# Optimization experiments

Measured on AMD Instinct MI355X. Metric: run time of the kernel, lower is better.

The kernel has to match this reference:

```python
import jax, jax.numpy as jnp
import numpy as np

D_MODEL = 1024
N_HEADS = 16
SEQ = 2048
BATCH = 2
EPS = 1e-5


def layer_norm(x, g, b):
    mu = jnp.mean(x, axis=-1, keepdims=True)
    var = jnp.mean(jnp.square(x - mu), axis=-1, keepdims=True)
    return (x - mu) * jax.lax.rsqrt(var + EPS) * g + b


def setup_inputs() -> dict:
    key = jax.random.key(0)
    ks = jax.random.split(key, 10)
    D = D_MODEL
    s = lambda fan_in: 1.0 / np.sqrt(fan_in)
    return {
        "x": jax.random.normal(ks[0], (BATCH, SEQ, D), dtype=jnp.float32),
        # weights stored [in, out] (torch Linear is y = x @ W.T; equivalent math)
        "w_attn": jax.random.uniform(ks[1], (D, 3 * D), minval=-s(D), maxval=s(D), dtype=jnp.float32),
        "b_attn": jnp.zeros((3 * D,), jnp.float32),
        "w_proj": jax.random.uniform(ks[2], (D, D), minval=-s(D), maxval=s(D), dtype=jnp.float32),
        "b_proj": jnp.zeros((D,), jnp.float32),
        "ln1_g": jnp.ones((D,), jnp.float32),
        "ln1_b": jnp.zeros((D,), jnp.float32),
        "ln2_g": jnp.ones((D,), jnp.float32),
        "ln2_b": jnp.zeros((D,), jnp.float32),
        "w_fc1": jax.random.uniform(ks[3], (D, 4 * D), minval=-s(D), maxval=s(D), dtype=jnp.float32),
        "b_fc1": jnp.zeros((4 * D,), jnp.float32),
        "w_fc2": jax.random.uniform(ks[4], (4 * D, D), minval=-s(4 * D), maxval=s(4 * D), dtype=jnp.float32),
        "b_fc2": jnp.zeros((D,), jnp.float32),
    }


def reference(x, w_attn, b_attn, w_proj, b_proj, ln1_g, ln1_b, ln2_g, ln2_b, w_fc1, b_fc1, w_fc2, b_fc2):
    B, L, D = x.shape
    H = N_HEADS
    Dh = D // H

    # --- attention sublayer ---
    h = layer_norm(x, ln1_g, ln1_b)
    qkv = h @ w_attn + b_attn                      # [B, L, 3D]
    # SOURCE BUG (faithful): q, k, v are all taken from the k third.
    k = qkv[..., D:2 * D]
    kh = k.reshape(B, L, H, Dh).transpose(0, 2, 1, 3)   # [B, H, L, Dh]
    att = jnp.einsum('bhqd,bhkd->bhqk', kh, kh) / jnp.sqrt(jnp.float32(Dh))
    att = jax.nn.softmax(att, axis=-1)
    out = jnp.einsum('bhqk,bhkd->bhqd', att, kh)         # [B, H, L, Dh]
    out = out.transpose(0, 2, 1, 3).reshape(B, L, D)
    x = x + (out @ w_proj + b_proj)

    # --- feed-forward sublayer ---
    h = layer_norm(x, ln2_g, ln2_b)
    h = jax.nn.relu(h @ w_fc1 + b_fc1)
    x = x + (h @ w_fc2 + b_fc2)
    return x
```

## Files before the change

kernel.cpp:

```cpp
#include <hip/hip_runtime.h>


typedef __attribute__((ext_vector_type(8))) short s8v;
typedef __attribute__((ext_vector_type(4))) short s4v;
typedef __attribute__((ext_vector_type(4))) float f4v;

#define D_MODEL 1024
#define SEQ 2048
#define BATCH 2
#define NH 16
#define DH 64
#define MROWS (BATCH * SEQ)

#define KH_SCALE 0.42466088f
#define KH_ISCALE 2.3548200f

__device__ __forceinline__ float b2f(unsigned short u) {
  union { unsigned int i; float f; } v; v.i = ((unsigned int)u) << 16; return v.f;
}
__device__ __forceinline__ unsigned short f2b(float f) {
  unsigned int i = __builtin_bit_cast(unsigned int, f);
  unsigned int r = (i + 0x7fffu + ((i >> 16) & 1u)) >> 16;
  return (unsigned short)r;
}
__device__ __forceinline__ void async16(const void* g, void* l) {
  __builtin_amdgcn_global_load_lds(
      (const __attribute__((address_space(1))) unsigned int*)g,
      (__attribute__((address_space(3))) unsigned int*)l, 16, 0, 0);
}
__device__ __forceinline__ unsigned short cvt_b(float f) { return f2b(f); }
__device__ __forceinline__ unsigned short cvt_b(unsigned short u) { return u; }

__device__ __forceinline__ float xp2(float x) {
#if __has_builtin(__builtin_amdgcn_exp2f)
  return __builtin_amdgcn_exp2f(x);
#else
  return exp2f(x);
#endif
}

__device__ __forceinline__ s4v cvt4(float a, float b, float c, float d) {
  unsigned int lo, hi;
  asm("v_cvt_pk_bf16_f32 %0, %1, %2" : "=v"(lo) : "v"(a), "v"(b));
  asm("v_cvt_pk_bf16_f32 %0, %1, %2" : "=v"(hi) : "v"(c), "v"(d));
  union { unsigned long long u; s4v v; } u;
  u.u = ((unsigned long long)hi << 32) | (unsigned long long)lo;
  return u.v;
}

#if __has_builtin(__builtin_amdgcn_mfma_f32_16x16x16_bf16)
__device__ __forceinline__ f4v mfma16(s4v a, s4v b, f4v c) {
  return __builtin_amdgcn_mfma_f32_16x16x16_bf16(a, b, c, 0, 0, 0);
}
#elif __has_builtin(__builtin_amdgcn_mfma_f32_16x16x16bf16_1k)
__device__ __forceinline__ f4v mfma16(s4v a, s4v b, f4v c) {
  return __builtin_amdgcn_mfma_f32_16x16x16bf16_1k(a, b, c, 0, 0, 0);
}
#else
__device__ __forceinline__ f4v mfma16(s4v a, s4v b, f4v c) {
  s8v aa = {a[0], a[1], a[2], a[3], 0, 0, 0, 0};
  s8v bb = {b[0], b[1], b[2], b[3], 0, 0, 0, 0};
  return __builtin_amdgcn_mfma_f32_16x16x32_bf16(aa, bb, c, 0, 0, 0);
}
#endif

__device__ __forceinline__ int xcd_swz(int bidl, int nwg) {
  return (nwg & 7) ? bidl : ((bidl & 7) * (nwg >> 3) + (bidl >> 3));
}

__global__ __launch_bounds__(256) void ln_kernel(
    const float* __restrict__ x, const float* __restrict__ g,
    const float* __restrict__ bb, unsigned short* __restrict__ out) {
  int row = blockIdx.x;
  int t = threadIdx.x;
  const float* xr = x + (size_t)row * D_MODEL;
  float v[4];
  float s = 0.f, s2 = 0.f;
#pragma unroll
  for (int i = 0; i < 4; ++i) {
    float f = xr[t + 256 * i];
    v[i] = f; s += f; s2 += f * f;
  }
#pragma unroll
  for (int off = 1; off < 64; off <<= 1) {
    s += __shfl_xor(s, off, 64);
    s2 += __shfl_xor(s2, off, 64);
  }
  __shared__ float red[8];
  if ((t & 63) == 0) { red[t >> 6] = s; red[4 + (t >> 6)] = s2; }
  __syncthreads();
  s = red[0] + red[1] + red[2] + red[3];
  s2 = red[4] + red[5] + red[6] + red[7];
  float mu = s * (1.f / D_MODEL);
  float var = s2 * (1.f / D_MODEL) - mu * mu;
  float rstd = rsqrtf(var + 1e-5f);
#pragma unroll
  for (int i = 0; i < 4; ++i) {
    int c = t + 256 * i;
    float h = (v[i] - mu) * rstd * g[c] + bb[c];
    out[(size_t)row * D_MODEL + c] = f2b(h);
  }
}

template <typename T>
__global__ __launch_bounds__(256) void transpose_b(
    const T* __restrict__ src, unsigned short* __restrict__ dst,
    int srcStride, int dstStride, long long srcBatch, long long dstBatch) {
  __shared__ unsigned short tile[64][65];
  const T* s = src + (size_t)blockIdx.z * srcBatch;
  unsigned short* d = dst + (size_t)blockIdx.z * dstBatch;
  int n0 = blockIdx.x * 64, k0 = blockIdx.y * 64;
  for (int i = threadIdx.x; i < 4096; i += 256) {
    int k = i >> 6, n = i & 63;
    tile[k][n] = cvt_b(s[(size_t)(k0 + k) * srcStride + n0 + n]);
  }
  __syncthreads();
  for (int i = threadIdx.x; i < 4096; i += 256) {
    int n = i >> 6, k = i & 63;
    d[(size_t)(n0 + n) * dstStride + k0 + k] = tile[k][n];
  }
}

template <int RES, bool RELU, bool KH, int OUTF, int BM, int BN>
__global__ __launch_bounds__(256) void gemm_bt(
    const unsigned short* __restrict__ A, const unsigned short* __restrict__ Bt,
    const float* __restrict__ bias, const float* __restrict__ res,
    void* __restrict__ out, int M, int N, int K) {
  constexpr int MT = BM / 32;
  constexpr int NT = BN / 32;
  __shared__ __align__(16) unsigned short lsA[2][BM * 64];
  __shared__ __align__(16) unsigned short lsB[2][BN * 64];
  int tid = threadIdx.x;
  int lane = tid & 63, w = tid >> 6, quad = lane >> 4, l16 = lane & 15;
  int bidl = blockIdx.y * (int)gridDim.x + blockIdx.x;
  int swz = xcd_swz(bidl, (int)(gridDim.x * gridDim.y));
  int m0 = (swz / (int)gridDim.x) * BM, n0 = (swz % (int)gridDim.x) * BN;
  int wm = (w >> 1) * (BM / 2), wn = (w & 1) * (BN / 2);
  f4v acc[MT][NT] = {};

  auto stage = [&](int bsel, int ktE) {
#pragma unroll
    for (int i = 0; i < MT; ++i) {
      int cb = w * (BM * 2) + i * 64;
      int ci = cb + lane;
      int row = ci >> 3, c = ci & 7;
      int cs = c ^ (row & 7);
      async16(A + (size_t)(m0 + row) * K + ktE + cs * 8, &lsA[bsel][cb * 8]);
    }
#pragma unroll
    for (int i = 0; i < NT; ++i) {
      int cb = w * (BN * 2) + i * 64;
      int ci = cb + lane;
      int row = ci >> 3, c = ci & 7;
      int cs = c ^ (row & 7);
      async16(Bt + (size_t)(n0 + row) * K + ktE + cs * 8, &lsB[bsel][cb * 8]);
    }
  };

  stage(0, 0);
  int nK = K >> 6;
  for (int kt = 0; kt < nK; ++kt) {
    int b = kt & 1;
    if (kt + 1 < nK) {
      stage(b ^ 1, (kt + 1) << 6);
      if constexpr (MT + NT == 4)      asm volatile("s_waitcnt vmcnt(4)" ::: "memory");
      else if constexpr (MT + NT == 6) asm volatile("s_waitcnt vmcnt(6)" ::: "memory");
      else                             asm volatile("s_waitcnt vmcnt(8)" ::: "memory");
    } else {
      asm volatile("s_waitcnt vmcnt(0)" ::: "memory");
    }
    __builtin_amdgcn_sched_barrier(0);
    __builtin_amdgcn_s_barrier();
    __builtin_amdgcn_sched_barrier(0);
#pragma unroll
    for (int s = 0; s < 2; ++s) {
      s8v af[MT], bf[NT];
#pragma unroll
      for (int t = 0; t < MT; ++t) {
        int am = wm + t * 16 + l16;
        int ac = (s * 4 + quad) ^ (am & 7);
        af[t] = *(const s8v*)(&lsA[b][am * 64 + ac * 8]);
      }
#pragma unroll
      for (int t = 0; t < NT; ++t) {
        int bn = wn + t * 16 + l16;
        int bc = (s * 4 + quad) ^ (bn & 7);
        bf[t] = *(const s8v*)(&lsB[b][bn * 64 + bc * 8]);
      }
#pragma unroll
      for (int ti = 0; ti < MT; ++ti)
#pragma unroll
        for (int tj = 0; tj < NT; ++tj)
          acc[ti][tj] = __builtin_amdgcn_mfma_f32_16x16x32_bf16(
              af[ti], bf[tj], acc[ti][tj], 0, 0, 0);
    }
    asm volatile("s_waitcnt lgkmcnt(0)" ::: "memory");
    __builtin_amdgcn_sched_barrier(0);
    __builtin_amdgcn_s_barrier();
    __builtin_amdgcn_sched_barrier(0);
  }
#pragma unroll
  for (int tj = 0; tj < NT; ++tj) {
    int col = n0 + wn + tj * 16 + l16;
    float bv = bias[col];
#pragma unroll
    for (int ti = 0; ti < MT; ++ti) {
#pragma unroll
      for (int r = 0; r < 4; ++r) {
        int rowg = m0 + wm + ti * 16 + quad * 4 + r;
        float vv = acc[ti][tj][r] + bv;
        if (KH) vv *= KH_SCALE;
        if (RES == 2) vv += res[(size_t)rowg * N + col];
        if (RELU) vv = fmaxf(vv, 0.f);
        size_t oidx;
        if (KH) {
          int b2 = rowg >> 11, l = rowg & 2047, h = col >> 6, d = col & 63;
          oidx = (((size_t)(b2 * NH + h)) * SEQ + l) * DH + d;
        } else {
          oidx = (size_t)rowg * N + col;
        }
        if (OUTF == 0) ((unsigned short*)out)[oidx] = f2b(vv);
        else           ((float*)out)[oidx] = vv;
      }
    }
  }
}

__global__ __launch_bounds__(512, 2) void gemm256(
    const unsigned short* __restrict__ A, const unsigned short* __restrict__ Bt,
    const float* __restrict__ bias, unsigned short* __restrict__ out,
    bool relu, int M, int N, int K) {
  __shared__ __align__(16) unsigned short lsA[2][2][128 * 64];
  __shared__ __align__(16) unsigned short lsB[2][2][128 * 64];
  int tid = threadIdx.x;
  int lane = tid & 63, w = tid >> 6, quad = lane >> 4, l16 = lane & 15;
  int wr = w >> 2, wc = w & 3;
  int bidl = blockIdx.y * (int)gridDim.x + blockIdx.x;
  int swz = xcd_swz(bidl, (int)(gridDim.x * gridDim.y));
  int m0 = (swz / (int)gridDim.x) * 256, n0 = (swz % (int)gridDim.x) * 256;
  f4v acc[8][4] = {};

  auto stageA = [&](int par, int h, int kt) {
#pragma unroll
    for (int i = 0; i < 2; ++i) {
      int cb = w * 128 + i * 64;
      int ci = cb + lane;
      int r = ci >> 3, c = ci & 7;
      int cs = c ^ (r & 7);
      int grow = ((r >> 6) << 7) + h * 64 + (r & 63);
      async16(A + (size_t)(m0 + grow) * K + kt * 64 + cs * 8,
              &lsA[par][h][cb * 8]);
    }
  };
  auto stageB = [&](int par, int h, int kt) {
#pragma unroll
    for (int i = 0; i < 2; ++i) {
      int cb = w * 128 + i * 64;
      int ci = cb + lane;
      int r = ci >> 3, c = ci & 7;
      int cs = c ^ (r & 7);
      int gn = ((r >> 5) << 6) + h * 32 + (r & 31);
      async16(Bt + (size_t)(n0 + gn) * K + kt * 64 + cs * 8,
              &lsB[par][h][cb * 8]);
    }
  };

#define PHASE(PAR, MH, NH, STAGE_STMT, VMN)                                    \
  {                                                                            \
    s8v af[4][2], bf[2][2];                                                    \
    _Pragma("unroll") for (int tm = 0; tm < 4; ++tm) {                         \
      int lr = wr * 64 + tm * 16 + l16;                                        \
      _Pragma("unroll") for (int s = 0; s < 2; ++s) {                          \
        int ac = (s * 4 + quad) ^ (lr & 7);                                    \
        af[tm][s] = *(const s8v*)(&lsA[PAR][MH][lr * 64 + ac * 8]);            \
      }                                                                        \
    }                                                                          \
    _Pragma("unroll") for (int tn = 0; tn < 2; ++tn) {                         \
      int rb = wc * 32 + tn * 16 + l16;                                        \
      _Pragma("unroll") for (int s = 0; s < 2; ++s) {                          \
        int bc = (s * 4 + quad) ^ (rb & 7);                                    \
        bf[tn][s] = *(const s8v*)(&lsB[PAR][NH][rb * 64 + bc * 8]);            \
      }                                                                        \
    }                                                                          \
    STAGE_STMT;                                                                \
    __builtin_amdgcn_sched_barrier(0);                                         \
    __builtin_amdgcn_s_barrier();                                              \
    __builtin_amdgcn_sched_barrier(0);                                         \
    __builtin_amdgcn_s_setprio(1);                                             \
    _Pragma("unroll") for (int s = 0; s < 2; ++s)                              \
      _Pragma("unroll") for (int tm = 0; tm < 4; ++tm)                         \
        _Pragma("unroll") for (int tn = 0; tn < 2; ++tn)                       \
          acc[MH * 4 + tm][NH * 2 + tn] =                                      \
              __builtin_amdgcn_mfma_f32_16x16x32_bf16(                         \
                  af[tm][s], bf[tn][s], acc[MH * 4 + tm][NH * 2 + tn], 0, 0, 0);\
    __builtin_amdgcn_s_setprio(0);                                             \
    __builtin_amdgcn_sched_barrier(0);                                         \
    if (VMN == 4) { asm volatile("s_waitcnt vmcnt(4)" ::: "memory"); }         \
    else if (VMN == 0) { asm volatile("s_waitcnt vmcnt(0)" ::: "memory"); }    \
    __builtin_amdgcn_sched_barrier(0);                                         \
    __builtin_amdgcn_s_barrier();                                              \
    __builtin_amdgcn_sched_barrier(0);                                         \
  }

  int nT = K >> 6;
  stageA(0, 0, 0); stageB(0, 0, 0); stageA(0, 1, 0); stageB(0, 1, 0);
  stageB(1, 0, 1); stageA(1, 0, 1);
  asm volatile("s_waitcnt vmcnt(4)" ::: "memory");
  __builtin_amdgcn_sched_barrier(0);
  __builtin_amdgcn_s_barrier();
  __builtin_amdgcn_sched_barrier(0);

  for (int t = 0; t < nT; t += 2) {
    bool s2 = (t + 2) < nT, s3 = (t + 3) < nT;
    PHASE(0, 0, 0, { stageA(1, 1, t + 1); }, -1)
    PHASE(0, 1, 0, { stageB(1, 1, t + 1); }, -1)
    PHASE(0, 0, 1, { if (s2) stageB(0, 0, t + 2); }, -1)
    PHASE(0, 1, 1, { if (s2) stageA(0, 0, t + 2); }, (s2 ? 4 : 0))
    PHASE(1, 0, 0, { if (s2) stageA(0, 1, t + 2); }, -1)
    PHASE(1, 1, 0, { if (s2) stageB(0, 1, t + 2); }, -1)
    PHASE(1, 0, 1, { if (s3) stageB(1, 0, t + 3); }, -1)
    PHASE(1, 1, 1, { if (s3) stageA(1, 0, t + 3); }, (s3 ? 4 : 0))
  }
#undef PHASE

#pragma unroll
  for (int mi = 0; mi < 8; ++mi) {
    int mh = mi >> 2, tm = mi & 3;
#pragma unroll
    for (int nj = 0; nj < 4; ++nj) {
      int nh = nj >> 1, tn = nj & 1;
      int col = n0 + wc * 64 + nh * 32 + tn * 16 + l16;
      float bv = bias[col];
#pragma unroll
      for (int r = 0; r < 4; ++r) {
        int rowg = m0 + wr * 128 + mh * 64 + tm * 16 + quad * 4 + r;
        float vv = acc[mi][nj][r] + bv;
        if (relu) vv = fmaxf(vv, 0.f);
        out[(size_t)rowg * N + col] = f2b(vv);
      }
    }
  }
}

__global__ __launch_bounds__(256) void gemm_proj(
    const unsigned short* __restrict__ Opart, const float* __restrict__ lpart,
    const unsigned short* __restrict__ Bt, const float* __restrict__ bias,
    const float* __restrict__ res, float* __restrict__ out, int M, int N, int K) {
  __shared__ __align__(16) unsigned short lsA[2][64 * 64];
  __shared__ __align__(16) unsigned short lsB[2][64 * 64];
  int tid = threadIdx.x;
  int lane = tid & 63, w = tid >> 6, quad = lane >> 4, l16 = lane & 15;
  int bidl = blockIdx.y * (int)gridDim.x + blockIdx.x;
  int swz = xcd_swz(bidl, (int)(gridDim.x * gridDim.y));
  int m0 = (swz / (int)gridDim.x) * 64, n0 = (swz % (int)gridDim.x) * 64;
  int wm = (w >> 1) * 32, wn = (w & 1) * 32;
  f4v acc[2][2] = {};

  int ci_[2], csA[2], mA[2], b2A[2], lA[2];
#pragma unroll
  for (int i = 0; i < 2; ++i) {
    int cb = w * 128 + i * 64;
    int ci = cb + lane;
    int row = ci >> 3, c = ci & 7;
    ci_[i] = ci; csA[i] = c ^ (row & 7);
    mA[i] = m0 + row; b2A[i] = mA[i] >> 11; lA[i] = mA[i] & 2047;
  }
  s8v o0r[2], o1r[2];
  float lsr0[2], lsr1[2];
  auto issueA = [&](int kt) {
#pragma unroll
    for (int i = 0; i < 2; ++i) {
      const unsigned short* pa =
          Opart + (size_t)mA[i] * D_MODEL + kt * 64 + csA[i] * 8;
      o0r[i] = *(const s8v*)pa;
      o1r[i] = *(const s8v*)(pa + (size_t)MROWS * D_MODEL);
      size_t lidx = ((size_t)b2A[i] * NH + kt) * SEQ + lA[i];
      lsr0[i] = lpart[lidx];
      lsr1[i] = lpart[(size_t)BATCH * NH * SEQ + lidx];
    }
  };
  auto issueB = [&](int bsel, int ktE) {
#pragma unroll
    for (int i = 0; i < 2; ++i) {
      int cb = w * 128 + i * 64;
      int ci = cb + lane;
      int row = ci >> 3, c = ci & 7;
      int cs = c ^ (row & 7);
      async16(Bt + (size_t)(n0 + row) * K + ktE + cs * 8, &lsB[bsel][cb * 8]);
    }
  };
  auto combineWrite = [&](int bsel) {
#pragma unroll
    for (int i = 0; i < 2; ++i) {
      float inv = KH_ISCALE / (lsr0[i] + lsr1[i]);
      float f[8];
#pragma unroll
      for (int j = 0; j < 8; ++j)
        f[j] = (b2f((unsigned short)o0r[i][j]) +
                b2f((unsigned short)o1r[i][j])) * inv;
      s4v lo = cvt4(f[0], f[1], f[2], f[3]);
      s4v hi = cvt4(f[4], f[5], f[6], f[7]);
      s8v vv = {lo[0], lo[1], lo[2], lo[3], hi[0], hi[1], hi[2], hi[3]};
      *(s8v*)(&lsA[bsel][ci_[i] * 8]) = vv;
    }
  };

  issueA(0); issueB(0, 0);
  __builtin_amdgcn_sched_barrier(0);
  asm volatile("s_waitcnt vmcnt(2)" ::: "memory");
  __builtin_amdgcn_sched_barrier(0);
  combineWrite(0);
  asm volatile("s_waitcnt lgkmcnt(0)" ::: "memory");
  __builtin_amdgcn_sched_barrier(0);

  int nK = K >> 6;
  for (int kt = 0; kt < nK; ++kt) {
    int b = kt & 1;
    if (kt + 1 < nK) {
      issueA(kt + 1); issueB(b ^ 1, (kt + 1) << 6);
      __builtin_amdgcn_sched_barrier(0);
      asm volatile("s_waitcnt vmcnt(10)" ::: "memory");
    } else {
      __builtin_amdgcn_sched_barrier(0);
      asm volatile("s_waitcnt vmcnt(0)" ::: "memory");
    }
    __builtin_amdgcn_sched_barrier(0);
    __builtin_amdgcn_s_barrier();
    __builtin_amdgcn_sched_barrier(0);
#pragma unroll
    for (int s = 0; s < 2; ++s) {
      s8v af[2], bf[2];
#pragma unroll
      for (int t = 0; t < 2; ++t) {
        int am = wm + t * 16 + l16;
        int ac = (s * 4 + quad) ^ (am & 7);
        af[t] = *(const s8v*)(&lsA[b][am * 64 + ac * 8]);
      }
#pragma unroll
      for (int t = 0; t < 2; ++t) {
        int bn = wn + t * 16 + l16;
        int bc = (s * 4 + quad) ^ (bn & 7);
        bf[t] = *(const s8v*)(&lsB[b][bn * 64 + bc * 8]);
      }
#pragma unroll
      for (int ti = 0; ti < 2; ++ti)
#pragma unroll
        for (int tj = 0; tj < 2; ++tj)
          acc[ti][tj] = __builtin_amdgcn_mfma_f32_16x16x32_bf16(
              af[ti], bf[tj], acc[ti][tj], 0, 0, 0);
    }
    if (kt + 1 < nK) {
      __builtin_amdgcn_sched_barrier(0);
      asm volatile("s_waitcnt vmcnt(2)" ::: "memory");
      __builtin_amdgcn_sched_barrier(0);
      combineWrite(b ^ 1);
    }
    asm volatile("s_waitcnt lgkmcnt(0)" ::: "memory");
    __builtin_amdgcn_sched_barrier(0);
    __builtin_amdgcn_s_barrier();
    __builtin_amdgcn_sched_barrier(0);
  }
#pragma unroll
  for (int tj = 0; tj < 2; ++tj) {
    int col = n0 + wn + tj * 16 + l16;
    float bv = bias[col];
#pragma unroll
    for (int ti = 0; ti < 2; ++ti) {
#pragma unroll
      for (int r = 0; r < 4; ++r) {
        int rowg = m0 + wm + ti * 16 + quad * 4 + r;
        float vv = acc[ti][tj][r] + bv + res[(size_t)rowg * N + col];
        out[(size_t)rowg * N + col] = vv;
      }
    }
  }
}

__global__ __launch_bounds__(256) void flash_k(
    const unsigned short* __restrict__ kh, const unsigned short* __restrict__ khT,
    unsigned short* __restrict__ Opart, float* __restrict__ lpart) {
  __shared__ __align__(16) unsigned short lsK[128 * 64];
  __shared__ __align__(16) unsigned short lsKT[64 * 128];
  int tid = threadIdx.x;
  int lane = tid & 63, w = tid >> 6, quad = lane >> 4, l16 = lane & 15;
  int split = blockIdx.x, bh = blockIdx.y, qb = blockIdx.z;
  const unsigned short* khB = kh + (size_t)bh * SEQ * DH;
  const unsigned short* khTB = khT + (size_t)bh * DH * SEQ;
  unsigned short* Op = Opart + (size_t)split * MROWS * D_MODEL;
  float* lp = lpart + (size_t)split * BATCH * NH * SEQ;
  s8v aQ[2][2];
#pragma unroll
  for (int g = 0; g < 2; ++g) {
    int q = qb * 128 + w * 32 + g * 16 + l16;
#pragma unroll
    for (int s = 0; s < 2; ++s)
      aQ[g][s] = *(const s8v*)(khB + (size_t)q * DH + s * 32 + quad * 8);
  }
  const s4v vone = {(short)0x3F80, (short)0x3F80, (short)0x3F80, (short)0x3F80};
  f4v accO[2][4] = {};
  f4v accL[2] = {};

  for (int kt8 = 0; kt8 < 8; ++kt8) {
    int key0 = split * 1024 + kt8 * 128;
#pragma unroll
    for (int i = 0; i < 4; ++i) {
      int cb = w * 256 + i * 64;
      int ci = cb + lane;
      int row = ci >> 3, c = ci & 7;
      int cs = c ^ (row & 7);
      async16(khB + (size_t)(key0 + row) * DH + cs * 8, &lsK[cb * 8]);
    }
#pragma unroll
    for (int i = 0; i < 4; ++i) {
      int cb = w * 256 + i * 64;
      int ci = cb + lane;
      int row = ci >> 4, c = ci & 15;
      int cs = c ^ (row & 15);
      async16(khTB + (size_t)row * SEQ + key0 + cs * 8, &lsKT[cb * 8]);
    }
    __builtin_amdgcn_s_waitcnt(0x0f70);
    __syncthreads();
#pragma unroll
    for (int half = 0; half < 2; ++half) {
      f4v accST[2][4] = {};
#pragma unroll
      for (int s = 0; s < 2; ++s) {
#pragma unroll
        for (int tj = 0; tj < 4; ++tj) {
          int key = half * 64 + tj * 16 + l16;
          int c = (s * 4 + quad) ^ (key & 7);
          s8v kf = *(const s8v*)(&lsK[key * 64 + c * 8]);
#pragma unroll
          for (int g = 0; g < 2; ++g)
            accST[g][tj] = __builtin_amdgcn_mfma_f32_16x16x32_bf16(
                kf, aQ[g][s], accST[g][tj], 0, 0, 0);
        }
      }
#pragma unroll
      for (int tj = 0; tj < 4; ++tj) {
        s4v pf[2];
#pragma unroll
        for (int g = 0; g < 2; ++g) {
          float p0 = xp2(accST[g][tj][0]);
          float p1 = xp2(accST[g][tj][1]);
          float p2 = xp2(accST[g][tj][2]);
          float p3 = xp2(accST[g][tj][3]);
          pf[g] = cvt4(p0, p1, p2, p3);
          accL[g] = mfma16(pf[g], vone, accL[g]);
        }
#pragma unroll
        for (int db = 0; db < 4; ++db) {
          int d = db * 16 + l16;
          int ch = (half * 8 + tj * 2 + (quad >> 1)) ^ (d & 15);
          s4v vf = *(const s4v*)(&lsKT[d * 128 + ch * 8 + (quad & 1) * 4]);
#pragma unroll
          for (int g = 0; g < 2; ++g)
            accO[g][db] = mfma16(pf[g], vf, accO[g][db]);
        }
      }
    }
    __syncthreads();
  }
  int b = bh >> 4, h = bh & 15;
#pragma unroll
  for (int g = 0; g < 2; ++g) {
    if (l16 == 0) {
#pragma unroll
      for (int r = 0; r < 4; ++r) {
        int q = qb * 128 + w * 32 + g * 16 + quad * 4 + r;
        lp[(size_t)bh * SEQ + q] = accL[g][r];
      }
    }
#pragma unroll
    for (int r = 0; r < 4; ++r) {
      int l = qb * 128 + w * 32 + g * 16 + quad * 4 + r;
#pragma unroll
      for (int db = 0; db < 4; ++db) {
        int d = db * 16 + l16;
        Op[((size_t)(b * SEQ + l)) * D_MODEL + h * DH + d] = f2b(accO[g][db][r]);
      }
    }
  }
}

extern "C" void kernel_launch(void* const* d_in, const int* in_sizes, int n_in,
                              void* d_out, int out_size, void* d_ws, size_t ws_size,
                              hipStream_t stream) {
  (void)in_sizes; (void)n_in; (void)out_size;
  const float* x      = (const float*)d_in[0];
  const float* w_attn = (const float*)d_in[1];
  const float* b_attn = (const float*)d_in[2];
  const float* w_proj = (const float*)d_in[3];
  const float* b_proj = (const float*)d_in[4];
  const float* ln1_g  = (const float*)d_in[5];
  const float* ln1_b  = (const float*)d_in[6];
  const float* ln2_g  = (const float*)d_in[7];
  const float* ln2_b  = (const float*)d_in[8];
  const float* w_fc1  = (const float*)d_in[9];
  const float* b_fc1  = (const float*)d_in[10];
  const float* w_fc2  = (const float*)d_in[11];
  const float* b_fc2  = (const float*)d_in[12];

  char* ws = (char*)d_ws;
  unsigned short* Opart = (unsigned short*)ws;
  unsigned short* kh    = (unsigned short*)(ws + (size_t)(16u << 20));
  unsigned short* khT   = (unsigned short*)(ws + (size_t)(24u << 20));
  float*          x1    = (float*)(ws + (size_t)(32u << 20));
  unsigned short* hbuf  = (unsigned short*)(ws + (size_t)(48u << 20));
  float*          lpart = (float*)(ws + (size_t)(48u << 20));
  float* outf = (float*)d_out;
  bool big_ws = ws_size >= ((size_t)72u << 20);

  unsigned short* wTk;
  unsigned short* wTp;
  unsigned short* wTf1;
  unsigned short* wTf2;
  unsigned short* fc1o;
  if (big_ws) {
    wTk  = (unsigned short*)(ws + (size_t)(56u << 20));
    wTp  = wTk;
    wTf1 = wTk;
    wTf2 = (unsigned short*)(ws + (size_t)(64u << 20));
    fc1o = (unsigned short*)ws;
  } else {
    wTk  = (unsigned short*)ws;
    wTp  = kh;
    wTf1 = (unsigned short*)ws;
    wTf2 = (unsigned short*)(ws + (size_t)(8u << 20));
    fc1o = kh;
  }

  dim3 blk(256);
  hipLaunchKernelGGL(ln_kernel, dim3(MROWS), blk, 0, stream, x, ln1_g, ln1_b, hbuf);
  hipLaunchKernelGGL(transpose_b<float>, dim3(16, 16, 1), blk, 0, stream,
                     w_attn + 1024, wTk, 3 * D_MODEL, D_MODEL, 0LL, 0LL);
  hipLaunchKernelGGL((gemm_bt<0, false, true, 0, 64, 64>), dim3(16, 64), blk, 0,
                     stream, hbuf, wTk, b_attn + 1024, nullptr, (void*)kh,
                     MROWS, D_MODEL, D_MODEL);
  hipLaunchKernelGGL(transpose_b<unsigned short>, dim3(1, 32, 32), blk, 0, stream,
                     kh, khT, DH, SEQ, (long long)(SEQ * DH), (long long)(DH * SEQ));
  hipLaunchKernelGGL(flash_k, dim3(2, 32, SEQ / 128), blk, 0, stream,
                     kh, khT, Opart, lpart);
  hipLaunchKernelGGL(transpose_b<float>, dim3(16, 16, 1), blk, 0, stream,
                     w_proj, wTp, D_MODEL, D_MODEL, 0LL, 0LL);
  hipLaunchKernelGGL(gemm_proj, dim3(16, 64), blk, 0, stream,
                     Opart, lpart, wTp, b_proj, x, x1,
                     MROWS, D_MODEL, D_MODEL);
  hipLaunchKernelGGL(ln_kernel, dim3(MROWS), blk, 0, stream, x1, ln2_g, ln2_b, hbuf);
  hipLaunchKernelGGL(transpose_b<float>, dim3(64, 16, 1), blk, 0, stream,
                     w_fc1, wTf1, 4 * D_MODEL, D_MODEL, 0LL, 0LL);
  hipLaunchKernelGGL(transpose_b<float>, dim3(16, 64, 1), blk, 0, stream,
                     w_fc2, wTf2, D_MODEL, 4 * D_MODEL, 0LL, 0LL);
  if (big_ws) {
    hipLaunchKernelGGL(gemm256, dim3(16, 16), dim3(512), 0, stream,
                       hbuf, wTf1, b_fc1, fc1o, true,
                       MROWS, 4 * D_MODEL, D_MODEL);
    hipLaunchKernelGGL((gemm_bt<2, false, false, 1, 64, 64>), dim3(16, 64), blk, 0,
                       stream, fc1o, wTf2, b_fc2, x1, (void*)outf,
                       MROWS, D_MODEL, 4 * D_MODEL);
  } else {
    for (int c = 0; c < 2; ++c) {
      const unsigned short* h2c = hbuf + (size_t)c * 2048 * D_MODEL;
      const float* x1c = x1 + (size_t)c * 2048 * D_MODEL;
      float* outc = outf + (size_t)c * 2048 * D_MODEL;
      hipLaunchKernelGGL((gemm_bt<0, true, false, 0, 128, 64>), dim3(64, 16), blk, 0,
                         stream, h2c, wTf1, b_fc1, nullptr, (void*)fc1o,
                         2048, 4 * D_MODEL, D_MODEL);
      hipLaunchKernelGGL((gemm_bt<2, false, false, 1, 64, 64>), dim3(16, 32), blk, 0,
                         stream, fc1o, wTf2, b_fc2, x1c, (void*)outc,
                         2048, D_MODEL, 4 * D_MODEL);
    }
  }
}
```

Before: 331.4 us.

## Use LDS transpose reads in flash kernel, drop khT transpose, double-buffer K

Removes the separate transposed-K buffer and its transpose kernel launch. V fragments are now read from the single K tile in LDS with ds_read_b64_tr_b16. K tiles are double-buffered with async loads, so the next tile's fetch overlaps compute. The row-sum MFMA is merged into one 16x16x32 per two tiles. The cost is hand-placed waitcnt and sched barriers, and a new LDS layout without XOR swizzle that may bank-conflict.

```diff
diff --git a/kernel.cpp b/kernel.cpp
--- a/kernel.cpp
+++ b/kernel.cpp
@@ -63,6 +63,13 @@
   return __builtin_amdgcn_mfma_f32_16x16x32_bf16(aa, bb, c, 0, 0, 0);
 }
 #endif
+
+typedef __attribute__((address_space(3))) const unsigned short* lds_cp;
+__device__ __forceinline__ s4v tr16(lds_cp p) {
+  unsigned long long d;
+  asm volatile("ds_read_b64_tr_b16 %0, %1" : "=v"(d) : "v"(p));
+  return __builtin_bit_cast(s4v, d);
+}
 
 __device__ __forceinline__ int xcd_swz(int bidl, int nwg) {
   return (nwg & 7) ? bidl : ((bidl & 7) * (nwg >> 3) + (bidl >> 3));
@@ -477,15 +484,13 @@
 }
 
 __global__ __launch_bounds__(256) void flash_k(
-    const unsigned short* __restrict__ kh, const unsigned short* __restrict__ khT,
+    const unsigned short* __restrict__ kh,
     unsigned short* __restrict__ Opart, float* __restrict__ lpart) {
-  __shared__ __align__(16) unsigned short lsK[128 * 64];
-  __shared__ __align__(16) unsigned short lsKT[64 * 128];
+  __shared__ __align__(16) unsigned short lsK[2][8192];
   int tid = threadIdx.x;
   int lane = tid & 63, w = tid >> 6, quad = lane >> 4, l16 = lane & 15;
   int split = blockIdx.x, bh = blockIdx.y, qb = blockIdx.z;
   const unsigned short* khB = kh + (size_t)bh * SEQ * DH;
-  const unsigned short* khTB = khT + (size_t)bh * DH * SEQ;
   unsigned short* Op = Opart + (size_t)split * MROWS * D_MODEL;
   float* lp = lpart + (size_t)split * BATCH * NH * SEQ;
   s8v aQ[2][2];
@@ -496,30 +501,35 @@
     for (int s = 0; s < 2; ++s)
       aQ[g][s] = *(const s8v*)(khB + (size_t)q * DH + s * 32 + quad * 8);
   }
-  const s4v vone = {(short)0x3F80, (short)0x3F80, (short)0x3F80, (short)0x3F80};
+  const s8v vone8 = {(short)0x3F80, (short)0x3F80, (short)0x3F80, (short)0x3F80,
+                     (short)0x3F80, (short)0x3F80, (short)0x3F80, (short)0x3F80};
   f4v accO[2][4] = {};
   f4v accL[2] = {};
 
+  auto stageK = [&](int bsel, int key0) {
+#pragma unroll
+    for (int i = 0; i < 4; ++i) {
+      int ci = w * 256 + i * 64 + lane;
+      async16(khB + (size_t)(key0 + ((ci >> 1) & 127)) * DH +
+                  (ci >> 8) * 16 + (ci & 1) * 8,
+              &lsK[bsel][(w * 256 + i * 64) * 8]);
+    }
+  };
+  lds_cp ls0 = (lds_cp)&lsK[0][0];
+  lds_cp trb = ls0 + quad * 64 + l16 * 4;
+
+  stageK(0, split * 1024);
   for (int kt8 = 0; kt8 < 8; ++kt8) {
-    int key0 = split * 1024 + kt8 * 128;
-#pragma unroll
-    for (int i = 0; i < 4; ++i) {
-      int cb = w * 256 + i * 64;
-      int ci = cb + lane;
-      int row = ci >> 3, c = ci & 7;
-      int cs = c ^ (row & 7);
-      async16(khB + (size_t)(key0 + row) * DH + cs * 8, &lsK[cb * 8]);
-    }
-#pragma unroll
-    for (int i = 0; i < 4; ++i) {
-      int cb = w * 256 + i * 64;
-      int ci = cb + lane;
-      int row = ci >> 4, c = ci & 15;
-      int cs = c ^ (row & 15);
-      async16(khTB + (size_t)row * SEQ + key0 + cs * 8, &lsKT[cb * 8]);
-    }
-    __builtin_amdgcn_s_waitcnt(0x0f70);
-    __syncthreads();
+    int b = kt8 & 1;
+    if (kt8 + 1 < 8) {
+      stageK(b ^ 1, split * 1024 + (kt8 + 1) * 128);
+      asm volatile("s_waitcnt vmcnt(4)" ::: "memory");
+    } else {
+      asm volatile("s_waitcnt vmcnt(0)" ::: "memory");
+    }
+    __builtin_amdgcn_sched_barrier(0);
+    __builtin_amdgcn_s_barrier();
+    __builtin_amdgcn_sched_barrier(0);
 #pragma unroll
     for (int half = 0; half < 2; ++half) {
       f4v accST[2][4] = {};
@@ -527,17 +537,22 @@
       for (int s = 0; s < 2; ++s) {
 #pragma unroll
         for (int tj = 0; tj < 4; ++tj) {
-          int key = half * 64 + tj * 16 + l16;
-          int c = (s * 4 + quad) ^ (key & 7);
-          s8v kf = *(const s8v*)(&lsK[key * 64 + c * 8]);
+          s8v kf = *(const s8v*)(&lsK[b][(2 * s + (quad >> 1)) * 2048 +
+                                         (half * 64 + tj * 16 + l16) * 16 +
+                                         (quad & 1) * 8]);
 #pragma unroll
           for (int g = 0; g < 2; ++g)
             accST[g][tj] = __builtin_amdgcn_mfma_f32_16x16x32_bf16(
                 kf, aQ[g][s], accST[g][tj], 0, 0, 0);
         }
       }
+      s4v pprev[2];
 #pragma unroll
       for (int tj = 0; tj < 4; ++tj) {
+        s4v vt[4];
+#pragma unroll
+        for (int db = 0; db < 4; ++db)
+          vt[db] = tr16(trb + b * 8192 + db * 2048 + half * 1024 + tj * 256);
         s4v pf[2];
 #pragma unroll
         for (int g = 0; g < 2; ++g) {
@@ -546,20 +561,32 @@
           float p2 = xp2(accST[g][tj][2]);
           float p3 = xp2(accST[g][tj][3]);
           pf[g] = cvt4(p0, p1, p2, p3);
-          accL[g] = mfma16(pf[g], vone, accL[g]);
         }
-#pragma unroll
-        for (int db = 0; db < 4; ++db) {
-          int d = db * 16 + l16;
-          int ch = (half * 8 + tj * 2 + (quad >> 1)) ^ (d & 15);
-          s4v vf = *(const s4v*)(&lsKT[d * 128 + ch * 8 + (quad & 1) * 4]);
+        if (tj & 1) {
+#pragma unroll
+          for (int g = 0; g < 2; ++g) {
+            s8v pp = {pprev[g][0], pprev[g][1], pprev[g][2], pprev[g][3],
+                      pf[g][0], pf[g][1], pf[g][2], pf[g][3]};
+            accL[g] = __builtin_amdgcn_mfma_f32_16x16x32_bf16(
+                pp, vone8, accL[g], 0, 0, 0);
+          }
+        } else {
+#pragma unroll
+          for (int g = 0; g < 2; ++g) pprev[g] = pf[g];
+        }
+        asm volatile("s_waitcnt lgkmcnt(0)" ::: "memory");
+        __builtin_amdgcn_sched_barrier(0);
+#pragma unroll
+        for (int db = 0; db < 4; ++db)
 #pragma unroll
           for (int g = 0; g < 2; ++g)
-            accO[g][db] = mfma16(pf[g], vf, accO[g][db]);
-        }
-      }
-    }
-    __syncthreads();
+            accO[g][db] = mfma16(pf[g], vt[db], accO[g][db]);
+      }
+    }
+    asm volatile("s_waitcnt lgkmcnt(0)" ::: "memory");
+    __builtin_amdgcn_sched_barrier(0);
+    __builtin_amdgcn_s_barrier();
+    __builtin_amdgcn_sched_barrier(0);
   }
   int b = bh >> 4, h = bh & 15;
 #pragma unroll
@@ -604,7 +631,6 @@
   char* ws = (char*)d_ws;
   unsigned short* Opart = (unsigned short*)ws;
   unsigned short* kh    = (unsigned short*)(ws + (size_t)(16u << 20));
-  unsigned short* khT   = (unsigned short*)(ws + (size_t)(24u << 20));
   float*          x1    = (float*)(ws + (size_t)(32u << 20));
   unsigned short* hbuf  = (unsigned short*)(ws + (size_t)(48u << 20));
   float*          lpart = (float*)(ws + (size_t)(48u << 20));
@@ -624,7 +650,7 @@
     fc1o = (unsigned short*)ws;
   } else {
     wTk  = (unsigned short*)ws;
-    wTp  = kh;
+    wTp  = (unsigned short*)(ws + (size_t)(24u << 20));
     wTf1 = (unsigned short*)ws;
     wTf2 = (unsigned short*)(ws + (size_t)(8u << 20));
     fc1o = kh;
@@ -637,10 +663,8 @@
   hipLaunchKernelGGL((gemm_bt<0, false, true, 0, 64, 64>), dim3(16, 64), blk, 0,
                      stream, hbuf, wTk, b_attn + 1024, nullptr, (void*)kh,
                      MROWS, D_MODEL, D_MODEL);
-  hipLaunchKernelGGL(transpose_b<unsigned short>, dim3(1, 32, 32), blk, 0, stream,
-                     kh, khT, DH, SEQ, (long long)(SEQ * DH), (long long)(DH * SEQ));
   hipLaunchKernelGGL(flash_k, dim3(2, 32, SEQ / 128), blk, 0, stream,
-                     kh, khT, Opart, lpart);
+                     kh, Opart, lpart);
   hipLaunchKernelGGL(transpose_b<float>, dim3(16, 16, 1), blk, 0, stream,
                      w_proj, wTp, D_MODEL, D_MODEL, 0LL, 0LL);
   hipLaunchKernelGGL(gemm_proj, dim3(16, 64), blk, 0, stream,
```

After: 321.1 us. 1.03x faster.
